# Optimization experiments

Hardware: AMD Instinct MI355X
Metric: run time of the kernel (lower is better)

Reference implementation:

```python
import jax, jax.numpy as jnp
import numpy as np

DIM = 512      # dim
H = 8          # num_heads
NV = 3         # num_view
KC = 75        # k (cls tokens per view)
VS = 196       # voxel_size == N
QL = NV * KC   # 225 cls tokens total
EPS = 1e-5     # BatchNorm eps


def setup_inputs() -> dict:
    key = jax.random.key(0)
    ks = jax.random.split(key, 16)
    lin = lambda k, shape: jax.random.normal(k, shape, jnp.float32) * 0.02
    inp = {}
    inp['x'] = jax.random.normal(ks[0], (4, VS + QL, DIM), jnp.float32)
    # cross-attention projections (qkv_bias=False)
    inp['Wq'] = lin(ks[1], (DIM, DIM))
    inp['Wk'] = lin(ks[2], (DIM, DIM))
    inp['Wv'] = lin(ks[3], (DIM, DIM))
    # output projection (has bias)
    inp['Wproj'] = lin(ks[4], (DIM, DIM)); inp['bproj'] = jnp.zeros((DIM,), jnp.float32)
    # conv_ffn: depthwise 3x3, BN, relu, depthwise 3x3, BN, relu, 1x1 conv (all bias-free)
    inp['dw1'] = lin(ks[5], (DIM, 1, 3, 3))
    inp['dw2'] = lin(ks[6], (DIM, 1, 3, 3))
    inp['pw'] = lin(ks[7], (DIM, DIM))  # 1x1 conv weight (O, C)
    inp['bn1_g'] = jnp.ones((DIM,), jnp.float32); inp['bn1_b'] = jnp.zeros((DIM,), jnp.float32)
    inp['bn1_m'] = jnp.zeros((DIM,), jnp.float32); inp['bn1_v'] = jnp.ones((DIM,), jnp.float32)
    inp['bn2_g'] = jnp.ones((DIM,), jnp.float32); inp['bn2_b'] = jnp.zeros((DIM,), jnp.float32)
    inp['bn2_m'] = jnp.zeros((DIM,), jnp.float32); inp['bn2_v'] = jnp.ones((DIM,), jnp.float32)
    # MAB linears (bias=True), ln=False
    inp['mWq'] = lin(ks[8], (DIM, DIM)); inp['mbq'] = jnp.zeros((DIM,), jnp.float32)
    inp['mWk'] = lin(ks[9], (DIM, DIM)); inp['mbk'] = jnp.zeros((DIM,), jnp.float32)
    inp['mWv'] = lin(ks[10], (DIM, DIM)); inp['mbv'] = jnp.zeros((DIM,), jnp.float32)
    inp['mWo'] = lin(ks[11], (DIM, DIM)); inp['mbo'] = jnp.zeros((DIM,), jnp.float32)
    return inp


def _bn(x, g, b, m, v):
    # eval-mode BatchNorm2d over NCHW
    s = (g / jnp.sqrt(v + EPS))
    return (x - m[None, :, None, None]) * s[None, :, None, None] + b[None, :, None, None]


def _dw(x, w):
    # depthwise 3x3 conv, stride 1, SAME padding, groups = C
    return jax.lax.conv_general_dilated(
        x, w, (1, 1), 'SAME', feature_group_count=x.shape[1],
        dimension_numbers=('NCHW', 'OIHW', 'NCHW'))


def reference(x, Wq, Wk, Wv, Wproj, bproj, dw1, dw2, pw,
              bn1_g, bn1_b, bn1_m, bn1_v, bn2_g, bn2_b, bn2_m, bn2_v,
              mWq, mbq, mWk, mbk, mWv, mbv, mWo, mbo):
    B = x.shape[0]
    C = DIM
    hd = C // H
    cls_cat = x[:, -QL:, :]          # (B, Q, C)
    sem = x[:, :-QL, :]              # (B, N, C)
    N = sem.shape[1]
    scale = hd ** -0.5
    q = (cls_cat @ Wq.T).reshape(B, QL, H, hd) * scale   # (B,Q,H,hd)
    k = (sem @ Wk.T).reshape(B, N, H, hd)
    v = (sem @ Wv.T).reshape(B, N, H, hd)
    attn = jax.nn.softmax(jnp.einsum('bqhd,bnhd->bhqn', q, k), axis=-1)
    # degenerate per-position outer product: hs[b,n,q,h,d] = attn[b,h,q,n] * v[b,n,h,d]
    hs = jnp.einsum('bhqn,bnhd->bnqhd', attn, v).reshape(B, N, QL, C)
    h = hs.transpose(0, 3, 1, 2)     # (B, C, N, Q)
    h = jax.nn.relu(_bn(_dw(h, dw1), bn1_g, bn1_b, bn1_m, bn1_v))
    h = jax.nn.relu(_bn(_dw(h, dw2), bn2_g, bn2_b, bn2_m, bn2_v))
    h = jnp.einsum('bcnq,oc->bonq', h, pw)   # 1x1 conv
    # AvgPool2d(kernel=(N,1)) over the N axis -> (B, Q, C)
    cls_new = jnp.mean(h, axis=2).transpose(0, 2, 1)
    kc = cls_cat + cls_new
    # MAB(sem, kc): heads split along channels, scale = sqrt(dim_V) (full dim)
    Qm = (sem @ mWq.T + mbq).reshape(B, N, H, hd)
    Km = (kc @ mWk.T + mbk).reshape(B, QL, H, hd)
    Vm = (kc @ mWv.T + mbv).reshape(B, QL, H, hd)
    A = jax.nn.softmax(jnp.einsum('bnhd,bqhd->bhnq', Qm, Km) / np.sqrt(C).astype(np.float32), axis=-1)
    O = (Qm + jnp.einsum('bhnq,bqhd->bnhd', A, Vm)).reshape(B, N, C)
    O = O + jax.nn.relu(O @ mWo.T + mbo)
    return O @ Wproj.T + bproj       # (B, N, C)
```

## Files before the change

kernel.cpp:

```cpp
#include <hip/hip_runtime.h>
#include <math.h>

#define DIM 512
#define HEADS 8
#define QL 225
#define VS 196
#define BATCH 4
#define EPS_BN 1e-5f

typedef __attribute__((ext_vector_type(8))) short bf16x8;
typedef __attribute__((ext_vector_type(4))) float f32x4;
typedef __attribute__((ext_vector_type(2))) float f32x2;

__device__ __forceinline__ f32x2 pk_fma(f32x2 a, f32x2 b, f32x2 c) {
    return __builtin_elementwise_fma(a, b, c);
}
__device__ __forceinline__ f32x2 pk_mul(f32x2 a, f32x2 b) { return a * b; }
__device__ __forceinline__ f32x2 pk_add(f32x2 a, f32x2 b) { return a + b; }
__device__ __forceinline__ f32x2 pk_max0(f32x2 a) {
    f32x2 z = {0.f, 0.f};
    return __builtin_elementwise_max(a, z);
}
__device__ __forceinline__ float bperm(int idx, float v) {
    return __int_as_float(__builtin_amdgcn_ds_bpermute(idx, __float_as_int(v)));
}

__device__ __forceinline__ unsigned cvt_pk_bf16(float lo, float hi) {
    unsigned r;
    asm("v_cvt_pk_bf16_f32 %0, %1, %2" : "=v"(r) : "v"(lo), "v"(hi));
    return r;
}
__device__ __forceinline__ uint4 ld_cvt8(const float* p) {
    float4 x = *(const float4*)p;
    float4 y = *(const float4*)(p + 4);
    uint4 r;
    r.x = cvt_pk_bf16(x.x, x.y);
    r.y = cvt_pk_bf16(x.z, x.w);
    r.z = cvt_pk_bf16(y.x, y.y);
    r.w = cvt_pk_bf16(y.z, y.w);
    return r;
}
__device__ __forceinline__ uint4 ld_cvt8s(const float* p, const float* p2) {
    float4 x = *(const float4*)p;
    float4 y = *(const float4*)(p + 4);
    if (p2) {
        float4 x2 = *(const float4*)p2;
        float4 y2 = *(const float4*)(p2 + 4);
        x.x += x2.x; x.y += x2.y; x.z += x2.z; x.w += x2.w;
        y.x += y2.x; y.y += y2.y; y.z += y2.z; y.w += y2.w;
    }
    uint4 r;
    r.x = cvt_pk_bf16(x.x, x.y);
    r.y = cvt_pk_bf16(x.z, x.w);
    r.z = cvt_pk_bf16(y.x, y.y);
    r.w = cvt_pk_bf16(y.z, y.w);
    return r;
}

struct GJob {
    const float* A; const float* W; const float* bias; const float* Add; float* Out;
    const float* A2lo; const float* A2hi;
    long aBS, aOff, addBS, addOff;
    int aRows, addRows, M, relu;
    float scale; int a2split; int pad1, pad2;
};
struct GJobs { GJob j[4]; };

template<int LAYER>
__global__ __launch_bounds__(256) void gemm_multi(GJobs jobs) {
    const GJob J = jobs.j[blockIdx.z];
    const int bm = blockIdx.y * 32, bn = blockIdx.x * 32;
    if (bm >= J.M) return;
    __shared__ __align__(16) ushort As[32][72];
    __shared__ __align__(16) ushort Bs[32][72];
    const int tid = threadIdx.x;
    const int srow = tid >> 3, skq = tid & 7;
    const float *ap = nullptr, *ap2 = nullptr;
    {
        int m0 = bm + srow;
        if (m0 < J.M) {
            int bb = m0 / J.aRows; int r = m0 - bb * J.aRows;
            ap = J.A + bb * J.aBS + J.aOff + (long)r * 512 + skq * 8;
            if (J.A2lo) {
                ap2 = (m0 < J.a2split ? J.A2lo + (long)m0 * 512
                                      : J.A2hi + (long)(m0 - J.a2split) * 512) + skq * 8;
            }
        }
    }
    const float* bp = J.W + (long)(bn + srow) * 512 + skq * 8;

    const int lane = tid & 63, wid = tid >> 6;
    const int wr = wid >> 1, wc = wid & 1;
    const int lr = lane & 15, kg = lane >> 4;

    f32x4 acc = {};

    uint4 a01 = {0u,0u,0u,0u};
    if (ap) a01 = ld_cvt8s(ap, ap2);
    uint4 b01 = ld_cvt8(bp);

    for (int kt = 0; kt < 512; kt += 64) {
        __syncthreads();
        *(uint4*)&As[srow][skq * 8] = a01;
        *(uint4*)&Bs[srow][skq * 8] = b01;
        __syncthreads();
        if (kt + 64 < 512) {
            if (ap) a01 = ld_cvt8s(ap + kt + 64, ap2 ? ap2 + kt + 64 : nullptr);
            b01 = ld_cvt8(bp + kt + 64);
        }
        bf16x8 a0 = *(const bf16x8*)&As[wr * 16 + lr][kg * 8];
        bf16x8 a1 = *(const bf16x8*)&As[wr * 16 + lr][32 + kg * 8];
        bf16x8 b0 = *(const bf16x8*)&Bs[wc * 16 + lr][kg * 8];
        bf16x8 b1 = *(const bf16x8*)&Bs[wc * 16 + lr][32 + kg * 8];
        acc = __builtin_amdgcn_mfma_f32_16x16x32_bf16(a0, b0, acc, 0, 0, 0);
        acc = __builtin_amdgcn_mfma_f32_16x16x32_bf16(a1, b1, acc, 0, 0, 0);
    }

#pragma unroll
    for (int r = 0; r < 4; r++) {
        int m = bm + wr * 16 + kg * 4 + r;
        if (m >= J.M) continue;
        const float* addrow = nullptr;
        if (J.Add) {
            int bb2 = m / J.addRows; int rr = m - bb2 * J.addRows;
            addrow = J.Add + bb2 * J.addBS + J.addOff + (long)rr * 512;
        }
        int n = bn + wc * 16 + lr;
        float v = acc[r] * J.scale;
        if (J.bias) v += J.bias[n];
        if (J.relu) v = fmaxf(v, 0.f);
        if (addrow) v += addrow[n];
        J.Out[(long)m * 512 + n] = v;
    }
}

__global__ __launch_bounds__(256) void attn1_mfma(const float* __restrict__ qs,
                                                  const float* __restrict__ ks,
                                                  float* __restrict__ P) {
    int bid = blockIdx.x;
    int qt = bid & 3;
    int h = (bid >> 2) & 7;
    int b = bid >> 5;
    int tid = threadIdx.x;
    int wave = tid >> 6, lane = tid & 63;
    int lr = lane & 15, kg = lane >> 4;
    __shared__ __align__(16) ushort Kb[208][72];
    __shared__ __align__(16) ushort Qb[64][72];
    const long qBase = ((long)(b * QL)) * DIM + h * 64;
    const long kBase = ((long)(b * VS)) * DIM + h * 64;
    {
        int r = tid >> 2, c0 = (tid & 3) * 16;
        int q = qt * 64 + r;
        uint4 lo = {0u,0u,0u,0u}, hi = {0u,0u,0u,0u};
        if (q < QL) {
            const float* s = qs + qBase + (long)q * DIM + c0;
            lo = ld_cvt8(s); hi = ld_cvt8(s + 8);
        }
        *(uint4*)&Qb[r][c0] = lo; *(uint4*)&Qb[r][c0 + 8] = hi;
    }
    {
        int c0 = (tid & 3) * 16;
#pragma unroll
        for (int i = 0; i < 4; i++) {
            int r = (tid >> 2) + 64 * i;
            if (r < 208) {
                uint4 lo = {0u,0u,0u,0u}, hi = {0u,0u,0u,0u};
                if (r < VS) {
                    const float* s = ks + kBase + (long)r * DIM + c0;
                    lo = ld_cvt8(s); hi = ld_cvt8(s + 8);
                }
                *(uint4*)&Kb[r][c0] = lo; *(uint4*)&Kb[r][c0 + 8] = hi;
            }
        }
    }
    __syncthreads();

    bf16x8 bq0 = *(const bf16x8*)&Qb[wave * 16 + lr][kg * 8];
    bf16x8 bq1 = *(const bf16x8*)&Qb[wave * 16 + lr][32 + kg * 8];
    f32x4 sc[13];
#pragma unroll
    for (int ct = 0; ct < 13; ct++) {
        bf16x8 a0 = *(const bf16x8*)&Kb[ct * 16 + lr][kg * 8];
        bf16x8 a1 = *(const bf16x8*)&Kb[ct * 16 + lr][32 + kg * 8];
        f32x4 z = {0.f, 0.f, 0.f, 0.f};
        z = __builtin_amdgcn_mfma_f32_16x16x32_bf16(a0, bq0, z, 0, 0, 0);
        z = __builtin_amdgcn_mfma_f32_16x16x32_bf16(a1, bq1, z, 0, 0, 0);
        sc[ct] = z;
    }
    float m = -1e30f;
#pragma unroll
    for (int ct = 0; ct < 13; ct++)
#pragma unroll
        for (int r = 0; r < 4; r++) {
            if (ct == 12 && kg > 0) sc[ct][r] = -1e30f;
            m = fmaxf(m, sc[ct][r]);
        }
    m = fmaxf(m, __shfl_xor(m, 16, 64));
    m = fmaxf(m, __shfl_xor(m, 32, 64));
    float s = 0.f;
#pragma unroll
    for (int ct = 0; ct < 13; ct++)
#pragma unroll
        for (int r = 0; r < 4; r++) {
            float e = expf(sc[ct][r] - m);
            sc[ct][r] = e;
            s += e;
        }
    s += __shfl_xor(s, 16, 64);
    s += __shfl_xor(s, 32, 64);
    float inv = 1.f / s;
    int q = qt * 64 + wave * 16 + lr;
    if (q < QL) {
        float* Pp = P + ((long)(b * HEADS + h)) * VS * QL + q;
#pragma unroll
        for (int ct = 0; ct < 13; ct++)
#pragma unroll
            for (int r = 0; r < 4; r++) {
                int n = ct * 16 + kg * 4 + r;
                if (n < VS) Pp[(long)n * QL] = sc[ct][r] * inv;
            }
    }
}

#define CSTEP8(N, PS, TAw,TAm2, TBw,TBm1, UAw,UAm2, UBw,UBm1)                      \
{                                                                                  \
    f32x2 vn = vcol2[(N)];                                                         \
    float psm = (PS) * qm;                                                         \
    f32x2 psm2 = {psm, psm};                                                       \
    f32x2 pv = pk_mul(psm2, vn);                                                   \
    f32x2 hm, hp;                                                                  \
    hm.x = bperm(upidx, pv.x); hm.y = bperm(upidx, pv.y);                          \
    hp.x = bperm(dnidx, pv.x); hp.y = bperm(dnidx, pv.y);                          \
    f32x2 g = z2;                                                                  \
    if ((N) >= 1 && (N) <= VS) {                                                   \
        f32x2 tC = pk_fma(hp, w1p[8], pk_fma(pv, w1p[7], pk_mul(hm, w1p[6])));     \
        f32x2 sg = pk_add(pk_add(tC, TBm1), pk_add(TAm2, b1v2));                   \
        g = pk_mul(pk_max0(sg), qm2);                                              \
    }                                                                              \
    TAw = pk_fma(hp, w1p[2], pk_fma(pv, w1p[1], pk_mul(hm, w1p[0])));              \
    TBw = pk_fma(hp, w1p[5], pk_fma(pv, w1p[4], pk_mul(hm, w1p[3])));              \
    f32x2 gm, gp;                                                                  \
    gm.x = bperm(upidx, g.x); gm.y = bperm(upidx, g.y);                            \
    gp.x = bperm(dnidx, g.x); gp.y = bperm(dnidx, g.y);                            \
    if ((N) >= alo && (N) <= ahi) {                                                \
        f32x2 uC = pk_fma(gp, w2p[8], pk_fma(g, w2p[7], pk_mul(gm, w2p[6])));      \
        f32x2 s2 = pk_add(pk_add(uC, UBm1), pk_add(UAm2, b2v2));                   \
        csum = pk_add(csum, pk_max0(s2));                                          \
    }                                                                              \
    UAw = pk_fma(gp, w2p[2], pk_fma(g, w2p[1], pk_mul(gm, w2p[0])));               \
    UBw = pk_fma(gp, w2p[5], pk_fma(g, w2p[4], pk_mul(gm, w2p[3])));               \
}

#define CBODY(N0, S0, S1, S2)                                                      \
    CSTEP8(N0,     S0, tAa,tAb, tBa,tBc, uAa,uAb, uBa,uBc)                         \
    CSTEP8((N0)+1, S1, tAb,tAc, tBb,tBa, uAb,uAc, uBb,uBa)                         \
    CSTEP8((N0)+2, S2, tAc,tAa, tBc,tBb, uAc,uAa, uBc,uBb)

__global__ __launch_bounds__(256) void conv_pk_kernel(
    const float* __restrict__ P, const float* __restrict__ vs,
    const float* __restrict__ dw1, const float* __restrict__ dw2,
    const float* __restrict__ bn1g, const float* __restrict__ bn1b,
    const float* __restrict__ bn1m, const float* __restrict__ bn1v,
    const float* __restrict__ bn2g, const float* __restrict__ bn2b,
    const float* __restrict__ bn2m, const float* __restrict__ bn2v,
    float* __restrict__ m2a, float* __restrict__ m2b1, float* __restrict__ m2b2) {
    int bc = blockIdx.x;
    int half = bc & 1;
    int c0 = ((bc >> 1) & 255) * 2;
    int b = bc >> 9;
    int h = c0 >> 6;
    const int no  = half ? 96 : 0;
    const int alo = half ? 100 : 2;
    const int ahi = half ? 197 : 99;
    int tid = threadIdx.x;
    int wave = tid >> 6, lane = tid & 63;
    int q = wave * 60 + lane - 2;
    bool outok = (lane >= 2 && lane <= 61 && q < QL);
    float qm = (q >= 0 && q < QL) ? 1.f : 0.f;
    f32x2 qm2 = {qm, qm};
    int qc = min(max(q, 0), QL - 1);
    const int upidx = ((lane - 1) & 63) << 2;
    const int dnidx = ((lane + 1) & 63) << 2;
    __shared__ __align__(8) f32x2 vcol2[200];
    if (tid < 200) {
        f32x2 t = {0.f, 0.f};
        if (tid < VS) {
            const float* vp = vs + ((long)(b * VS + tid)) * DIM + c0;
            t.x = vp[0]; t.y = vp[1];
        }
        vcol2[tid] = t;
    }
    float s1x = bn1g[c0]     * rsqrtf(bn1v[c0]     + EPS_BN);
    float s1y = bn1g[c0 + 1] * rsqrtf(bn1v[c0 + 1] + EPS_BN);
    float s2x = bn2g[c0]     * rsqrtf(bn2v[c0]     + EPS_BN);
    float s2y = bn2g[c0 + 1] * rsqrtf(bn2v[c0 + 1] + EPS_BN);
    f32x2 b1v2 = {bn1b[c0] - bn1m[c0] * s1x, bn1b[c0 + 1] - bn1m[c0 + 1] * s1y};
    f32x2 b2v2 = {bn2b[c0] - bn2m[c0] * s2x, bn2b[c0 + 1] - bn2m[c0 + 1] * s2y};
    f32x2 w1p[9], w2p[9];
#pragma unroll
    for (int i = 0; i < 9; i++) {
        w1p[i].x = dw1[c0 * 9 + i] * s1x;       w1p[i].y = dw1[(c0 + 1) * 9 + i] * s1y;
        w2p[i].x = dw2[c0 * 9 + i] * s2x;       w2p[i].y = dw2[(c0 + 1) * 9 + i] * s2y;
    }
    const float* Pp = P + ((long)(b * HEADS + h)) * VS * QL;
    const float* pqb = Pp + qc;
    __syncthreads();
    const f32x2 z2 = {0.f, 0.f};
    f32x2 tAa = z2, tAb = z2, tAc = z2, tBa = z2, tBb = z2, tBc = z2;
    f32x2 uAa = z2, uAb = z2, uAc = z2, uBa = z2, uBb = z2, uBc = z2;
    f32x2 csum = z2;
    float ps0 = pqb[(long)(no + 0) * QL];
    float ps1 = pqb[(long)(no + 1) * QL];
    float ps2v = pqb[(long)(no + 2) * QL];
    const float* pq = pqb + (long)(no + 3) * QL;
    for (int k = 0; k < 32; k++) {
        float pn0 = pq[0];
        float pn1 = pq[QL];
        float pn2 = pq[2 * QL];
        int N0 = no + k * 3;
        CBODY(N0, ps0, ps1, ps2v)
        ps0 = pn0; ps1 = pn1; ps2v = pn2;
        pq += 3 * QL;
    }
    float pt0 = (no + 99  < VS) ? pq[0]      : 0.f;
    float pt1 = (no + 100 < VS) ? pq[QL]     : 0.f;
    float pt2 = (no + 101 < VS) ? pq[2 * QL] : 0.f;
    { int N0 = no + 96; CBODY(N0, ps0, ps1, ps2v) }
    ps0 = pt0; ps1 = pt1; ps2v = pt2;
    { int N0 = no + 99; CBODY(N0, ps0, ps1, ps2v) }
    if (outok) {
        const float inv = 1.f / (float)VS;
        f32x2 o = csum * inv;
        int row = b * QL + q;
        if (!half) {
            *(f32x2*)&m2a[(long)row * 512 + c0] = o;
        } else {
            float* dst = (row < 784) ? (m2b1 + (long)row * 512) : (m2b2 + (long)(row - 784) * 512);
            *(f32x2*)&dst[c0] = o;
        }
    }
}

__global__ __launch_bounds__(256) void attn2_mfma(const float* __restrict__ Qm,
                                                  const float* __restrict__ Km,
                                                  const float* __restrict__ Vm,
                                                  float* __restrict__ O) {
    int bid = blockIdx.x;
    int nq = bid & 3;
    int h = (bid >> 2) & 7;
    int b = bid >> 5;
    int n0 = nq * 64;
    int tid = threadIdx.x;
    int wave = tid >> 6, lane = tid & 63;
    int lr = lane & 15, kg = lane >> 4;

    __shared__ __align__(16) char smem[77568];
    ushort (*VT)[264] = (ushort(*)[264])smem;
    ushort (*Qb)[72]  = (ushort(*)[72])(smem + 33792);
    ushort (*Kb)[72]  = (ushort(*)[72])(smem + 43008);
    ushort (*Pl)[264] = (ushort(*)[264])(smem + 33792);

    const long qmBase = ((long)(b * VS)) * DIM + h * 64;
    const long kmBase = ((long)(b * QL)) * DIM + h * 64;

    {
        int r = tid >> 2, c0 = (tid & 3) * 16;
        int n = min(n0 + r, VS - 1);
        const float* src = Qm + qmBase + (long)n * DIM + c0;
        *(uint4*)&Qb[r][c0]     = ld_cvt8(src);
        *(uint4*)&Qb[r][c0 + 8] = ld_cvt8(src + 8);
    }
    {
        int c0 = (tid & 3) * 16;
#pragma unroll
        for (int i = 0; i < 4; i++) {
            int r = (tid >> 2) + 64 * i;
            if (r < 240) {
                uint4 lo = {0u,0u,0u,0u}, hi = {0u,0u,0u,0u};
                if (r < QL) {
                    const float* src = Km + kmBase + (long)r * DIM + c0;
                    lo = ld_cvt8(src); hi = ld_cvt8(src + 8);
                }
                *(uint4*)&Kb[r][c0]     = lo;
                *(uint4*)&Kb[r][c0 + 8] = hi;
            }
        }
    }
    {
        int c0 = (tid & 3) * 16;
#pragma unroll
        for (int i = 0; i < 4; i++) {
            int qq = (tid >> 2) + 64 * i;
            if (qq < 240) {
                ushort u[16];
                if (qq < QL) {
                    const float* src = Vm + kmBase + (long)qq * DIM + c0;
                    *(uint4*)&u[0] = ld_cvt8(src);
                    *(uint4*)&u[8] = ld_cvt8(src + 8);
                } else {
#pragma unroll
                    for (int j = 0; j < 16; j++) u[j] = 0;
                }
#pragma unroll
                for (int j = 0; j < 16; j++) VT[c0 + j][qq] = u[j];
            }
        }
        int d = tid >> 2, qz = 240 + (tid & 3) * 4;
#pragma unroll
        for (int j = 0; j < 4; j++) VT[d][qz + j] = 0;
    }
    __syncthreads();

    bf16x8 a0 = *(const bf16x8*)&Qb[wave * 16 + lr][kg * 8];
    bf16x8 a1 = *(const bf16x8*)&Qb[wave * 16 + lr][32 + kg * 8];
    f32x4 sc[15];
#pragma unroll
    for (int ct = 0; ct < 15; ct++) {
        bf16x8 b0 = *(const bf16x8*)&Kb[ct * 16 + lr][kg * 8];
        bf16x8 b1 = *(const bf16x8*)&Kb[ct * 16 + lr][32 + kg * 8];
        f32x4 z = {0.f, 0.f, 0.f, 0.f};
        z = __builtin_amdgcn_mfma_f32_16x16x32_bf16(a0, b0, z, 0, 0, 0);
        z = __builtin_amdgcn_mfma_f32_16x16x32_bf16(a1, b1, z, 0, 0, 0);
        sc[ct] = z;
    }
    __syncthreads();

    const float scl = 0.044194173824159216f;
    float pinv[4];
#pragma unroll
    for (int r = 0; r < 4; r++) {
        float m = -1e30f;
#pragma unroll
        for (int ct = 0; ct < 15; ct++) {
            float v = sc[ct][r] * scl;
            if (ct * 16 + lr >= QL) v = -1e30f;
            sc[ct][r] = v;
            m = fmaxf(m, v);
        }
#pragma unroll
        for (int o = 1; o < 16; o <<= 1) m = fmaxf(m, __shfl_xor(m, o, 64));
        float s = 0.f;
#pragma unroll
        for (int ct = 0; ct < 15; ct++) {
            float e = expf(sc[ct][r] - m);
            sc[ct][r] = e;
            s += e;
        }
#pragma unroll
        for (int o = 1; o < 16; o <<= 1) s += __shfl_xor(s, o, 64);
        pinv[r] = 1.f / s;
    }
#pragma unroll
    for (int r = 0; r < 4; r++) {
        int row = wave * 16 + (lane >> 4) * 4 + r;
#pragma unroll
        for (int ct = 0; ct < 15; ct++) {
            float p = sc[ct][r] * pinv[r];
            Pl[row][ct * 16 + lr] = (ushort)(cvt_pk_bf16(p, p) & 0xffffu);
        }
        Pl[row][240 + lr] = 0;
    }
    __syncthreads();

    bf16x8 pa[8];
#pragma unroll
    for (int ks = 0; ks < 8; ks++)
        pa[ks] = *(const bf16x8*)&Pl[wave * 16 + lr][ks * 32 + kg * 8];
    f32x4 ov[4] = {};
#pragma unroll
    for (int dt = 0; dt < 4; dt++)
#pragma unroll
        for (int ks = 0; ks < 8; ks++) {
            bf16x8 vb = *(const bf16x8*)&VT[dt * 16 + lr][ks * 32 + kg * 8];
            ov[dt] = __builtin_amdgcn_mfma_f32_16x16x32_bf16(pa[ks], vb, ov[dt], 0, 0, 0);
        }

#pragma unroll
    for (int dt = 0; dt < 4; dt++)
#pragma unroll
        for (int r = 0; r < 4; r++) {
            int n = n0 + wave * 16 + (lane >> 4) * 4 + r;
            if (n < VS) {
                long addr = qmBase + (long)n * DIM + dt * 16 + lr;
                O[addr] = Qm[addr] + ov[dt][r];
            }
        }
}

static inline GJob mkjob(const float* A, int aRows, long aBS, long aOff,
                         const float* W, const float* bias,
                         const float* Add, int addRows, long addBS, long addOff,
                         float* Out, int M, float scale, int relu,
                         const float* A2lo = nullptr, const float* A2hi = nullptr,
                         int a2split = 0) {
    GJob j;
    j.A = A; j.W = W; j.bias = bias; j.Add = Add; j.Out = Out;
    j.A2lo = A2lo; j.A2hi = A2hi;
    j.aBS = aBS; j.aOff = aOff; j.addBS = addBS; j.addOff = addOff;
    j.aRows = aRows; j.addRows = addRows; j.M = M; j.relu = relu;
    j.scale = scale; j.a2split = a2split; j.pad1 = j.pad2 = 0;
    return j;
}

extern "C" void kernel_launch(void* const* d_in, const int* in_sizes, int n_in,
                              void* d_out, int out_size, void* d_ws, size_t ws_size,
                              hipStream_t stream) {
    const float* x     = (const float*)d_in[0];
    const float* Wq    = (const float*)d_in[1];
    const float* Wk    = (const float*)d_in[2];
    const float* Wv    = (const float*)d_in[3];
    const float* Wproj = (const float*)d_in[4];
    const float* bproj = (const float*)d_in[5];
    const float* dw1   = (const float*)d_in[6];
    const float* dw2   = (const float*)d_in[7];
    const float* pw    = (const float*)d_in[8];
    const float* bn1g  = (const float*)d_in[9];
    const float* bn1b  = (const float*)d_in[10];
    const float* bn1m  = (const float*)d_in[11];
    const float* bn1v  = (const float*)d_in[12];
    const float* bn2g  = (const float*)d_in[13];
    const float* bn2b  = (const float*)d_in[14];
    const float* bn2m  = (const float*)d_in[15];
    const float* bn2v  = (const float*)d_in[16];
    const float* mWq   = (const float*)d_in[17];
    const float* mbq   = (const float*)d_in[18];
    const float* mWk   = (const float*)d_in[19];
    const float* mbk   = (const float*)d_in[20];
    const float* mWv   = (const float*)d_in[21];
    const float* mbv   = (const float*)d_in[22];
    const float* mWo   = (const float*)d_in[23];
    const float* mbo   = (const float*)d_in[24];

    float* ws = (float*)d_ws;
    float* qs = ws;
    float* ks = ws + 460800;
    float* vsb = ws + 862208;
    float* P  = ws + 1263616;
    float* m2a = ws;
    float* m2b1 = ws + 460800;
    float* m2b2 = (float*)d_out;
    float* kc = ws + 1263616;
    float* Qm = ws + 1263616 + 460800;
    float* Vm = ws + 1263616 + 460800 + 401408;
    float* Km = ws;
    float* O  = ws + 460800;
    float* O2 = ws + 862208;

    const long xBS = 421L * DIM;
    const long clsOff = 196L * DIM;

    dim3 blk(256);

    {
        GJobs js;
        js.j[0] = mkjob(x, QL, xBS, clsOff, Wq, nullptr, nullptr, 1, 0, 0, qs, 900, 0.125f, 0);
        js.j[1] = mkjob(x, VS, xBS, 0, Wk, nullptr, nullptr, 1, 0, 0, ks, 784, 1.f, 0);
        js.j[2] = mkjob(x, VS, xBS, 0, Wv, nullptr, nullptr, 1, 0, 0, vsb, 784, 1.f, 0);
        js.j[3] = js.j[0];
        gemm_multi<0><<<dim3(16, 29, 3), blk, 0, stream>>>(js);
    }
    attn1_mfma<<<BATCH * HEADS * 4, blk, 0, stream>>>(qs, ks, P);
    conv_pk_kernel<<<2048, blk, 0, stream>>>(P, vsb, dw1, dw2,
                                             bn1g, bn1b, bn1m, bn1v,
                                             bn2g, bn2b, bn2m, bn2v, m2a, m2b1, m2b2);
    {
        GJobs js;
        js.j[0] = mkjob(m2a, 900, 0, 0, pw, nullptr, x, QL, xBS, clsOff, kc, 900, 1.f, 0,
                        m2b1, m2b2, 784);
        js.j[1] = mkjob(x, VS, xBS, 0, mWq, mbq, nullptr, 1, 0, 0, Qm, 784, 1.f, 0);
        js.j[2] = js.j[3] = js.j[0];
        gemm_multi<1><<<dim3(16, 29, 2), blk, 0, stream>>>(js);
    }
    {
        GJobs js;
        js.j[0] = mkjob(kc, 900, 0, 0, mWk, mbk, nullptr, 1, 0, 0, Km, 900, 1.f, 0);
        js.j[1] = mkjob(kc, 900, 0, 0, mWv, mbv, nullptr, 1, 0, 0, Vm, 900, 1.f, 0);
        js.j[2] = js.j[3] = js.j[0];
        gemm_multi<2><<<dim3(16, 29, 2), blk, 0, stream>>>(js);
    }
    attn2_mfma<<<BATCH * HEADS * 4, blk, 0, stream>>>(Qm, Km, Vm, O);
    {
        GJobs js;
        js.j[0] = mkjob(O, 784, 0, 0, mWo, mbo, O, 784, 0, 0, O2, 784, 1.f, 1);
        js.j[1] = js.j[2] = js.j[3] = js.j[0];
        gemm_multi<3><<<dim3(16, 25, 1), blk, 0, stream>>>(js);
    }
    {
        GJobs js;
        js.j[0] = mkjob(O2, 784, 0, 0, Wproj, bproj, nullptr, 1, 0, 0, (float*)d_out, 784, 1.f, 0);
        js.j[1] = js.j[2] = js.j[3] = js.j[0];
        gemm_multi<4><<<dim3(16, 25, 1), blk, 0, stream>>>(js);
    }
}
```

Baseline: 159.5 us.

## Replace ds_bpermute neighbor exchange with DPP row shifts in conv kernel

The depthwise-conv kernel used ds_bpermute to fetch the q-1 and q+1 neighbours across the 64-lane wave. It now uses DPP row_shr/row_shl, which only work inside 16-lane rows. To fit that, the q tiling changes to groups of 16 lanes that each produce 12 outputs with 2-lane halos, and the block grows to 320 threads to cover all 225 q values. DPP skips the LDS-path permute latency, but the larger halo ratio means more redundant lanes and more threads per block.

```diff
diff --git a/kernel.cpp b/kernel.cpp
--- a/kernel.cpp
+++ b/kernel.cpp
@@ -21,8 +21,11 @@
     f32x2 z = {0.f, 0.f};
     return __builtin_elementwise_max(a, z);
 }
-__device__ __forceinline__ float bperm(int idx, float v) {
-    return __int_as_float(__builtin_amdgcn_ds_bpermute(idx, __float_as_int(v)));
+__device__ __forceinline__ float dpp_lm(float v) {
+    return __int_as_float(__builtin_amdgcn_update_dpp(0, __float_as_int(v), 0x111, 0xF, 0xF, true));
+}
+__device__ __forceinline__ float dpp_lp(float v) {
+    return __int_as_float(__builtin_amdgcn_update_dpp(0, __float_as_int(v), 0x101, 0xF, 0xF, true));
 }
 
 __device__ __forceinline__ unsigned cvt_pk_bf16(float lo, float hi) {
@@ -222,15 +225,15 @@
     }
 }
 
-#define CSTEP8(N, PS, TAw,TAm2, TBw,TBm1, UAw,UAm2, UBw,UBm1)                      \
+#define CSTEP10(N, PS, TAw,TAm2, TBw,TBm1, UAw,UAm2, UBw,UBm1)                     \
 {                                                                                  \
     f32x2 vn = vcol2[(N)];                                                         \
     float psm = (PS) * qm;                                                         \
     f32x2 psm2 = {psm, psm};                                                       \
     f32x2 pv = pk_mul(psm2, vn);                                                   \
     f32x2 hm, hp;                                                                  \
-    hm.x = bperm(upidx, pv.x); hm.y = bperm(upidx, pv.y);                          \
-    hp.x = bperm(dnidx, pv.x); hp.y = bperm(dnidx, pv.y);                          \
+    hm.x = dpp_lm(pv.x); hm.y = dpp_lm(pv.y);                                      \
+    hp.x = dpp_lp(pv.x); hp.y = dpp_lp(pv.y);                                      \
     f32x2 g = z2;                                                                  \
     if ((N) >= 1 && (N) <= VS) {                                                   \
         f32x2 tC = pk_fma(hp, w1p[8], pk_fma(pv, w1p[7], pk_mul(hm, w1p[6])));     \
@@ -240,8 +243,8 @@
     TAw = pk_fma(hp, w1p[2], pk_fma(pv, w1p[1], pk_mul(hm, w1p[0])));              \
     TBw = pk_fma(hp, w1p[5], pk_fma(pv, w1p[4], pk_mul(hm, w1p[3])));              \
     f32x2 gm, gp;                                                                  \
-    gm.x = bperm(upidx, g.x); gm.y = bperm(upidx, g.y);                            \
-    gp.x = bperm(dnidx, g.x); gp.y = bperm(dnidx, g.y);                            \
+    gm.x = dpp_lm(g.x); gm.y = dpp_lm(g.y);                                        \
+    gp.x = dpp_lp(g.x); gp.y = dpp_lp(g.y);                                        \
     if ((N) >= alo && (N) <= ahi) {                                                \
         f32x2 uC = pk_fma(gp, w2p[8], pk_fma(g, w2p[7], pk_mul(gm, w2p[6])));      \
         f32x2 s2 = pk_add(pk_add(uC, UBm1), pk_add(UAm2, b2v2));                   \
@@ -252,11 +255,11 @@
 }
 
 #define CBODY(N0, S0, S1, S2)                                                      \
-    CSTEP8(N0,     S0, tAa,tAb, tBa,tBc, uAa,uAb, uBa,uBc)                         \
-    CSTEP8((N0)+1, S1, tAb,tAc, tBb,tBa, uAb,uAc, uBb,uBa)                         \
-    CSTEP8((N0)+2, S2, tAc,tAa, tBc,tBb, uAc,uAa, uBc,uBb)
-
-__global__ __launch_bounds__(256) void conv_pk_kernel(
+    CSTEP10(N0,     S0, tAa,tAb, tBa,tBc, uAa,uAb, uBa,uBc)                        \
+    CSTEP10((N0)+1, S1, tAb,tAc, tBb,tBa, uAb,uAc, uBb,uBa)                        \
+    CSTEP10((N0)+2, S2, tAc,tAa, tBc,tBb, uAc,uAa, uBc,uBb)
+
+__global__ __launch_bounds__(320) void conv_pk_kernel(
     const float* __restrict__ P, const float* __restrict__ vs,
     const float* __restrict__ dw1, const float* __restrict__ dw2,
     const float* __restrict__ bn1g, const float* __restrict__ bn1b,
@@ -273,14 +276,14 @@
     const int alo = half ? 100 : 2;
     const int ahi = half ? 197 : 99;
     int tid = threadIdx.x;
-    int wave = tid >> 6, lane = tid & 63;
-    int q = wave * 60 + lane - 2;
-    bool outok = (lane >= 2 && lane <= 61 && q < QL);
+    int lane = tid & 63;
+    int grp = tid >> 4;
+    int l = tid & 15;
+    int q = grp * 12 + l - 2;
+    bool outok = (l >= 2 && l <= 13 && q < QL);
     float qm = (q >= 0 && q < QL) ? 1.f : 0.f;
     f32x2 qm2 = {qm, qm};
     int qc = min(max(q, 0), QL - 1);
-    const int upidx = ((lane - 1) & 63) << 2;
-    const int dnidx = ((lane + 1) & 63) << 2;
     __shared__ __align__(8) f32x2 vcol2[200];
     if (tid < 200) {
         f32x2 t = {0.f, 0.f};
@@ -339,6 +342,7 @@
             *(f32x2*)&dst[c0] = o;
         }
     }
+    (void)lane;
 }
 
 __global__ __launch_bounds__(256) void attn2_mfma(const float* __restrict__ Qm,
@@ -560,9 +564,9 @@
         gemm_multi<0><<<dim3(16, 29, 3), blk, 0, stream>>>(js);
     }
     attn1_mfma<<<BATCH * HEADS * 4, blk, 0, stream>>>(qs, ks, P);
-    conv_pk_kernel<<<2048, blk, 0, stream>>>(P, vsb, dw1, dw2,
-                                             bn1g, bn1b, bn1m, bn1v,
-                                             bn2g, bn2b, bn2m, bn2v, m2a, m2b1, m2b2);
+    conv_pk_kernel<<<2048, dim3(320), 0, stream>>>(P, vsb, dw1, dw2,
+                                                   bn1g, bn1b, bn1m, bn1v,
+                                                   bn2g, bn2b, bn2m, bn2v, m2a, m2b1, m2b2);
     {
         GJobs js;
         js.j[0] = mkjob(m2a, 900, 0, 0, pw, nullptr, x, QL, xBS, clsOff, kc, 900, 1.f, 0,
```

Result: slower. 176.3 us (+10.5%).
